# Performance work log

Hardware: AMD Instinct MI355X
Metric: run time of the kernel (lower is better)

## Reference

```python
import jax, jax.numpy as jnp
import numpy as np

N_NODES = 100000
NEG_SLOPE = 0.2  # DGL GATConv default leaky_relu slope


def gat_layer(x, src, dst, W, attn_l, attn_r, bias):
    """One GATConv layer (DGL semantics). x: [N, F_in]; returns [N, H, D]."""
    H, D = attn_l.shape
    z = (x @ W).reshape(-1, H, D)                      # [N, H, D]
    el = jnp.einsum('nhd,hd->nh', z, attn_l)           # [N, H]
    er = jnp.einsum('nhd,hd->nh', z, attn_r)           # [N, H]
    e = jax.nn.leaky_relu(el[src] + er[dst], NEG_SLOPE)  # [E, H]
    # edge-softmax over incoming edges of each dst node
    m = jax.ops.segment_max(e, dst, num_segments=N_NODES)
    m = jnp.where(jnp.isfinite(m), m, 0.0)             # empty segments -> 0
    p = jnp.exp(e - m[dst])                            # [E, H]
    denom = jax.ops.segment_sum(p, dst, num_segments=N_NODES)
    alpha = p / jnp.maximum(denom[dst], 1e-9)          # [E, H]
    msg = z[src] * alpha[:, :, None]                   # [E, H, D]
    out = jax.ops.segment_sum(msg, dst, num_segments=N_NODES)
    return out + bias.reshape(1, H, D)


def setup_inputs() -> dict:
    key = jax.random.key(0)
    ks = jax.random.split(key, 10)
    in_dim, hidden, heads, out_dim, E = 500, 32, 4, 3, 1600000
    features = jax.random.normal(ks[0], (N_NODES, in_dim), dtype=jnp.float32)
    src = jax.random.randint(ks[1], (E,), 0, N_NODES, dtype=jnp.int64 if jax.config.jax_enable_x64 else jnp.int32)
    dst = jnp.sort(jax.random.randint(ks[2], (E,), 0, N_NODES, dtype=src.dtype))
    s1 = 1.0 / np.sqrt(in_dim)
    s2 = 1.0 / np.sqrt(hidden * heads)
    return {
        'features': features, 'src': src, 'dst': dst,
        'W1': jax.random.normal(ks[3], (in_dim, heads * hidden), dtype=jnp.float32) * s1,
        'al1': jax.random.normal(ks[4], (heads, hidden), dtype=jnp.float32) * s1,
        'ar1': jax.random.normal(ks[5], (heads, hidden), dtype=jnp.float32) * s1,
        'b1': jnp.zeros((heads * hidden,), dtype=jnp.float32),
        'W2': jax.random.normal(ks[6], (heads * hidden, out_dim), dtype=jnp.float32) * s2,
        'al2': jax.random.normal(ks[7], (1, out_dim), dtype=jnp.float32) * s2,
        'ar2': jax.random.normal(ks[8], (1, out_dim), dtype=jnp.float32) * s2,
        'b2': jnp.zeros((out_dim,), dtype=jnp.float32),
    }


def reference(features, src, dst, W1, al1, ar1, b1, W2, al2, ar2, b2):
    h = gat_layer(features, src, dst, W1, al1, ar1, b1)   # [N, H, hidden]
    h = jax.nn.elu(h.reshape(h.shape[0], -1))             # [N, H*hidden]
    h = gat_layer(h, src, dst, W2, al2, ar2, b2)          # [N, 1, out_dim]
    return h
```

## Files before the change

kernel.cpp:

```cpp
#include <hip/hip_runtime.h>
#include <hip/hip_fp16.h>
#include <math.h>

#define NNODES 100000
#define NEG_SLOPE 0.2f
#define FIN 500
#define KP 512
#define HID 128
#define NH 4
#define BMG 128

typedef __attribute__((ext_vector_type(8))) _Float16 half8v;
typedef __attribute__((ext_vector_type(4))) float f32x4;

__device__ __forceinline__ float lrelu(float x) { return x > 0.f ? x : NEG_SLOPE * x; }

__device__ __forceinline__ float sel4(float a0, float a1, float a2, float a3, int h) {
  float r = a0;
  r = (h == 1) ? a1 : r;
  r = (h == 2) ? a2 : r;
  r = (h == 3) ? a3 : r;
  return r;
}

__device__ __forceinline__ int tile_off(int col, int slot) {
  return col * 32 + ((slot ^ ((col >> 1) & 3)) << 3);
}

__global__ __launch_bounds__(256) void prep_kernel(const float* __restrict__ W1,
                                                   _Float16* __restrict__ BT_sw,
                                                   const int* __restrict__ dst, int E,
                                                   int* __restrict__ off) {
  int b = blockIdx.x;
  if (b < 256) {
    int p = b * 256 + threadIdx.x;
    int tile = p >> 12;
    int rem = p & 4095;
    int col = rem >> 5;
    int sw = (rem >> 3) & 3;
    int elem = rem & 7;
    int slot = sw ^ ((col >> 1) & 3);
    int k = tile * 32 + slot * 8 + elem;
    float v = (k < FIN) ? W1[k * HID + col] : 0.f;
    BT_sw[p] = (_Float16)v;
  } else {
    int n = (b - 256) * 256 + threadIdx.x;
    if (n > NNODES) return;
    int lo = 0, hi = E;
    while (lo < hi) {
      int mid = (lo + hi) >> 1;
      if (dst[mid] < n) lo = mid + 1; else hi = mid;
    }
    off[n] = lo;
  }
}

__global__ __launch_bounds__(256, 2) void gemm1_mfma_kernel(const float* __restrict__ A,
                                                            const _Float16* __restrict__ BT_sw,
                                                            const float* __restrict__ al,
                                                            const float* __restrict__ ar,
                                                            __half* __restrict__ z1h,
                                                            float* __restrict__ el,
                                                            float* __restrict__ er) {
  __shared__ __align__(16) float As[3][4096];
  __shared__ __align__(16) _Float16 Bsh[3][4096];

  const int t = threadIdx.x;
  const int w = t >> 6, lane = t & 63;
  const int fr = lane & 15, ko = lane >> 4;
  const int bm = blockIdx.x * BMG;

#define STAGE_A(BUF, S)                                                                     \
  do {                                                                                      \
    _Pragma("unroll")                                                                       \
    for (int j = 0; j < 4; j++) {                                                           \
      int c = j * 256 + w * 64 + lane;                                                      \
      int row = c >> 3, sl = c & 7;                                                         \
      int swz = sl ^ (row & 7);                                                             \
      const float* src = A + (size_t)min(bm + row, NNODES - 1) * FIN + (S) * 32 + swz * 4;  \
      __builtin_amdgcn_global_load_lds(                                                     \
          (const __attribute__((address_space(1))) unsigned int*)src,                       \
          (__attribute__((address_space(3))) unsigned int*)&As[BUF][c * 4], 16, 0, 0);      \
    }                                                                                       \
  } while (0)

#define STAGE_B(BUF, S)                                                                     \
  do {                                                                                      \
    _Pragma("unroll")                                                                       \
    for (int j = 0; j < 2; j++) {                                                           \
      int c = j * 256 + w * 64 + lane;                                                      \
      const _Float16* src = BT_sw + (size_t)(S) * 4096 + c * 8;                             \
      __builtin_amdgcn_global_load_lds(                                                     \
          (const __attribute__((address_space(1))) unsigned int*)src,                       \
          (__attribute__((address_space(3))) unsigned int*)&Bsh[BUF][c * 8], 16, 0, 0);     \
    }                                                                                       \
  } while (0)

  f32x4 acc[2][8];
#pragma unroll
  for (int i = 0; i < 2; i++)
#pragma unroll
    for (int j = 0; j < 8; j++) acc[i][j] = (f32x4){0.f, 0.f, 0.f, 0.f};

#define COMPUTE_STEP(BUF)                                                                   \
  do {                                                                                      \
    _Pragma("unroll")                                                                       \
    for (int mi = 0; mi < 2; mi++) {                                                        \
      int row = w * 32 + mi * 16 + fr;                                                      \
      int r7 = row & 7;                                                                     \
      const float* ap = &As[BUF][row * 32];                                                 \
      f32x4 a0 = *(const f32x4*)(ap + (((ko * 2) ^ r7) << 2));                              \
      f32x4 a1 = *(const f32x4*)(ap + (((ko * 2 + 1) ^ r7) << 2));                          \
      half8v af;                                                                            \
      _Pragma("unroll")                                                                     \
      for (int i = 0; i < 4; i++) {                                                         \
        af[i] = (_Float16)a0[i];                                                            \
        af[i + 4] = (_Float16)a1[i];                                                        \
      }                                                                                     \
      _Pragma("unroll")                                                                     \
      for (int ni = 0; ni < 8; ni++) {                                                      \
        half8v bf = *(half8v*)&Bsh[BUF][tile_off(ni * 16 + fr, ko)];                        \
        acc[mi][ni] = __builtin_amdgcn_mfma_f32_16x16x32_f16(af, bf, acc[mi][ni], 0, 0, 0); \
      }                                                                                     \
    }                                                                                       \
  } while (0)

  STAGE_A(0, 0);
  STAGE_B(0, 0);
  STAGE_A(1, 1);
  STAGE_B(1, 1);

#pragma unroll
  for (int s = 0; s < 16; ++s) {
    const int cb = s % 3;
    if (s <= 13) {
      asm volatile("s_waitcnt vmcnt(6)" ::: "memory");
    } else if (s == 14) {
      asm volatile("s_waitcnt vmcnt(2)" ::: "memory");
    } else {
      asm volatile("s_waitcnt vmcnt(0)" ::: "memory");
    }
    __builtin_amdgcn_sched_barrier(0);
    __builtin_amdgcn_s_barrier();
    __builtin_amdgcn_sched_barrier(0);
    if (s + 2 <= 14) {
      STAGE_A((s + 2) % 3, s + 2);
      STAGE_B((s + 2) % 3, s + 2);
    } else if (s + 2 == 15) {
      STAGE_B((s + 2) % 3, 15);
    }
    if (s < 15) {
      COMPUTE_STEP(cb);
    } else {
#pragma unroll
      for (int mi = 0; mi < 2; mi++) {
        int grow = min(bm + w * 32 + mi * 16 + fr, NNODES - 1);
        const float* pa = A + (size_t)grow * FIN;
        half8v af;
#pragma unroll
        for (int i = 0; i < 8; i++) {
          int k0 = 480 + ko * 8 + i;
          af[i] = (_Float16)((k0 < FIN) ? pa[k0] : 0.f);
        }
#pragma unroll
        for (int ni = 0; ni < 8; ni++) {
          half8v bf = *(half8v*)&Bsh[cb][tile_off(ni * 16 + fr, ko)];
          acc[mi][ni] = __builtin_amdgcn_mfma_f32_16x16x32_f16(af, bf, acc[mi][ni], 0, 0, 0);
        }
      }
    }
  }

#undef STAGE_A
#undef STAGE_B
#undef COMPUTE_STEP

  float alv[8], arv[8];
#pragma unroll
  for (int ni = 0; ni < 8; ni++) {
    alv[ni] = al[ni * 16 + fr];
    arv[ni] = ar[ni * 16 + fr];
  }
#pragma unroll
  for (int mi = 0; mi < 2; mi++) {
#pragma unroll
    for (int r = 0; r < 4; r++) {
      int grow = bm + w * 32 + mi * 16 + ko * 4 + r;
      bool ok = grow < NNODES;
      if (ok) {
#pragma unroll
        for (int ni = 0; ni < 8; ni++)
          z1h[(size_t)grow * HID + ni * 16 + fr] = __float2half(acc[mi][ni][r]);
      }
#pragma unroll
      for (int h = 0; h < 4; h++) {
        float cl = acc[mi][2 * h][r] * alv[2 * h] + acc[mi][2 * h + 1][r] * alv[2 * h + 1];
        float cr = acc[mi][2 * h][r] * arv[2 * h] + acc[mi][2 * h + 1][r] * arv[2 * h + 1];
#pragma unroll
        for (int m = 1; m <= 8; m <<= 1) {
          cl += __shfl_xor(cl, m);
          cr += __shfl_xor(cr, m);
        }
        if (fr == 0 && ok) {
          el[grow * NH + h] = cl;
          er[grow * NH + h] = cr;
        }
      }
    }
  }
}

__global__ __launch_bounds__(256) void gat1_agg_kernel(const __half* __restrict__ z1h,
                                                       const float* __restrict__ el,
                                                       const float* __restrict__ er,
                                                       const int* __restrict__ src,
                                                       const int* __restrict__ off,
                                                       const float* __restrict__ b1,
                                                       const float* __restrict__ W2,
                                                       const float* __restrict__ al2,
                                                       const float* __restrict__ ar2,
                                                       float4* __restrict__ z2el,
                                                       float* __restrict__ er2) {
  int wid = threadIdx.x >> 6, lane = threadIdx.x & 63;
  int n = blockIdx.x * 4 + wid;
  if (n >= NNODES) return;
  __shared__ float p_sh[4][64 * 4];

  int start = off[n], end = off[n + 1];
  const float4* el4 = reinterpret_cast<const float4*>(el);
  float4 er4 = reinterpret_cast<const float4*>(er)[n];

  const int g = lane >> 4;
  const int c4 = lane & 15;
  const int headc = c4 >> 2;
  float aA0 = 0.f, aA1 = 0.f, aA2 = 0.f, aA3 = 0.f;
  float aA4 = 0.f, aA5 = 0.f, aA6 = 0.f, aA7 = 0.f;
  float aB0 = 0.f, aB1 = 0.f, aB2 = 0.f, aB3 = 0.f;
  float aB4 = 0.f, aB5 = 0.f, aB6 = 0.f, aB7 = 0.f;
  float d0 = 0.f, d1 = 0.f, d2 = 0.f, d3 = 0.f;

  for (int base = start; base < end; base += 64) {
    int cnt = min(64, end - base);
    int sr = 0;
    float p0 = 0.f, p1 = 0.f, p2 = 0.f, p3 = 0.f;
    if (lane < cnt) {
      sr = src[base + lane];
      float4 x = el4[sr];
      p0 = __expf(lrelu(x.x + er4.x));
      p1 = __expf(lrelu(x.y + er4.y));
      p2 = __expf(lrelu(x.z + er4.z));
      p3 = __expf(lrelu(x.w + er4.w));
      d0 += p0; d1 += p1; d2 += p2; d3 += p3;
    }
    *(float4*)&p_sh[wid][lane * 4] = make_float4(p0, p1, p2, p3);
    __builtin_amdgcn_wave_barrier();
    for (int i = 0; i < cnt; i += 8) {
      int ea = i + g, eb = i + 4 + g;
      bool va_ = ea < cnt, vb_ = eb < cnt;
      int sa = __shfl(sr, va_ ? ea : 0);
      int sb = __shfl(sr, vb_ ? eb : 0);
      float pa = va_ ? p_sh[wid][ea * 4 + headc] : 0.f;
      float pb = vb_ ? p_sh[wid][eb * 4 + headc] : 0.f;
      uint4 ra = reinterpret_cast<const uint4*>(z1h + (size_t)sa * HID)[c4];
      uint4 rb = reinterpret_cast<const uint4*>(z1h + (size_t)sb * HID)[c4];
      float2 va0 = __half22float2(*(__half2*)&ra.x);
      float2 va1 = __half22float2(*(__half2*)&ra.y);
      float2 va2 = __half22float2(*(__half2*)&ra.z);
      float2 va3 = __half22float2(*(__half2*)&ra.w);
      aA0 = fmaf(pa, va0.x, aA0); aA1 = fmaf(pa, va0.y, aA1);
      aA2 = fmaf(pa, va1.x, aA2); aA3 = fmaf(pa, va1.y, aA3);
      aA4 = fmaf(pa, va2.x, aA4); aA5 = fmaf(pa, va2.y, aA5);
      aA6 = fmaf(pa, va3.x, aA6); aA7 = fmaf(pa, va3.y, aA7);
      float2 vb0 = __half22float2(*(__half2*)&rb.x);
      float2 vb1 = __half22float2(*(__half2*)&rb.y);
      float2 vb2 = __half22float2(*(__half2*)&rb.z);
      float2 vb3 = __half22float2(*(__half2*)&rb.w);
      aB0 = fmaf(pb, vb0.x, aB0); aB1 = fmaf(pb, vb0.y, aB1);
      aB2 = fmaf(pb, vb1.x, aB2); aB3 = fmaf(pb, vb1.y, aB3);
      aB4 = fmaf(pb, vb2.x, aB4); aB5 = fmaf(pb, vb2.y, aB5);
      aB6 = fmaf(pb, vb3.x, aB6); aB7 = fmaf(pb, vb3.y, aB7);
    }
    __builtin_amdgcn_wave_barrier();
  }

  float acc0 = aA0 + aB0, acc1 = aA1 + aB1, acc2 = aA2 + aB2, acc3 = aA3 + aB3;
  float acc4 = aA4 + aB4, acc5 = aA5 + aB5, acc6 = aA6 + aB6, acc7 = aA7 + aB7;

#pragma unroll
  for (int msk = 32; msk >= 1; msk >>= 1) {
    d0 += __shfl_xor(d0, msk);
    d1 += __shfl_xor(d1, msk);
    d2 += __shfl_xor(d2, msk);
    d3 += __shfl_xor(d3, msk);
  }
#pragma unroll
  for (int msk = 16; msk <= 32; msk <<= 1) {
    acc0 += __shfl_xor(acc0, msk); acc1 += __shfl_xor(acc1, msk);
    acc2 += __shfl_xor(acc2, msk); acc3 += __shfl_xor(acc3, msk);
    acc4 += __shfl_xor(acc4, msk); acc5 += __shfl_xor(acc5, msk);
    acc6 += __shfl_xor(acc6, msk); acc7 += __shfl_xor(acc7, msk);
  }

  if (g == 0) {
    float dh = sel4(d0, d1, d2, d3, headc);
    float inv = 1.f / fmaxf(dh, 1e-9f);
    float4 ba = reinterpret_cast<const float4*>(b1)[c4 * 2];
    float4 bb = reinterpret_cast<const float4*>(b1)[c4 * 2 + 1];
    float v0 = acc0 * inv + ba.x, v1 = acc1 * inv + ba.y;
    float v2 = acc2 * inv + ba.z, v3 = acc3 * inv + ba.w;
    float v4 = acc4 * inv + bb.x, v5 = acc5 * inv + bb.y;
    float v6 = acc6 * inv + bb.z, v7 = acc7 * inv + bb.w;
    v0 = v0 > 0.f ? v0 : __expf(v0) - 1.f;
    v1 = v1 > 0.f ? v1 : __expf(v1) - 1.f;
    v2 = v2 > 0.f ? v2 : __expf(v2) - 1.f;
    v3 = v3 > 0.f ? v3 : __expf(v3) - 1.f;
    v4 = v4 > 0.f ? v4 : __expf(v4) - 1.f;
    v5 = v5 > 0.f ? v5 : __expf(v5) - 1.f;
    v6 = v6 > 0.f ? v6 : __expf(v6) - 1.f;
    v7 = v7 > 0.f ? v7 : __expf(v7) - 1.f;
    const float* Wp = W2 + c4 * 8 * 3;
    float q0 = v0 * Wp[0] + v1 * Wp[3] + v2 * Wp[6] + v3 * Wp[9] +
               v4 * Wp[12] + v5 * Wp[15] + v6 * Wp[18] + v7 * Wp[21];
    float q1 = v0 * Wp[1] + v1 * Wp[4] + v2 * Wp[7] + v3 * Wp[10] +
               v4 * Wp[13] + v5 * Wp[16] + v6 * Wp[19] + v7 * Wp[22];
    float q2 = v0 * Wp[2] + v1 * Wp[5] + v2 * Wp[8] + v3 * Wp[11] +
               v4 * Wp[14] + v5 * Wp[17] + v6 * Wp[20] + v7 * Wp[23];
#pragma unroll
    for (int msk = 8; msk >= 1; msk >>= 1) {
      q0 += __shfl_xor(q0, msk);
      q1 += __shfl_xor(q1, msk);
      q2 += __shfl_xor(q2, msk);
    }
    if (c4 == 0) {
      z2el[n] = make_float4(q0, q1, q2, q0 * al2[0] + q1 * al2[1] + q2 * al2[2]);
      er2[n] = q0 * ar2[0] + q1 * ar2[1] + q2 * ar2[2];
    }
  }
}

__global__ __launch_bounds__(256) void gat2_agg_kernel(const float4* __restrict__ z2el,
                                                       const float* __restrict__ er2,
                                                       const int* __restrict__ src,
                                                       const int* __restrict__ off,
                                                       const float* __restrict__ b2,
                                                       float* __restrict__ out) {
  int wid = threadIdx.x >> 6, lane = threadIdx.x & 63;
  int n = blockIdx.x * 4 + wid;
  if (n >= NNODES) return;
  int start = off[n], end = off[n + 1];
  float ern = er2[n];
  float dA = 0.f, x0 = 0.f, x1 = 0.f, x2 = 0.f;
  float dB = 0.f, y0 = 0.f, y1 = 0.f, y2 = 0.f;
  int base = start + lane;
  for (; base + 64 < end; base += 128) {
    float4 za = z2el[src[base]];
    float4 zb = z2el[src[base + 64]];
    float pa = __expf(lrelu(za.w + ern));
    float pb = __expf(lrelu(zb.w + ern));
    dA += pa; dB += pb;
    x0 = fmaf(pa, za.x, x0); x1 = fmaf(pa, za.y, x1); x2 = fmaf(pa, za.z, x2);
    y0 = fmaf(pb, zb.x, y0); y1 = fmaf(pb, zb.y, y1); y2 = fmaf(pb, zb.z, y2);
  }
  if (base < end) {
    float4 za = z2el[src[base]];
    float pa = __expf(lrelu(za.w + ern));
    dA += pa;
    x0 = fmaf(pa, za.x, x0); x1 = fmaf(pa, za.y, x1); x2 = fmaf(pa, za.z, x2);
  }
  float d = dA + dB, a0 = x0 + y0, a1 = x1 + y1, a2 = x2 + y2;
#pragma unroll
  for (int msk = 32; msk >= 1; msk >>= 1) {
    a0 += __shfl_xor(a0, msk);
    a1 += __shfl_xor(a1, msk);
    a2 += __shfl_xor(a2, msk);
    d += __shfl_xor(d, msk);
  }
  if (lane == 0) {
    float inv = 1.f / fmaxf(d, 1e-9f);
    out[n * 3 + 0] = a0 * inv + b2[0];
    out[n * 3 + 1] = a1 * inv + b2[1];
    out[n * 3 + 2] = a2 * inv + b2[2];
  }
}

extern "C" void kernel_launch(void* const* d_in, const int* in_sizes, int n_in,
                              void* d_out, int out_size, void* d_ws, size_t ws_size,
                              hipStream_t stream) {
  const float* features = (const float*)d_in[0];
  const int* src = (const int*)d_in[1];
  const int* dst = (const int*)d_in[2];
  const float* W1 = (const float*)d_in[3];
  const float* al1 = (const float*)d_in[4];
  const float* ar1 = (const float*)d_in[5];
  const float* b1 = (const float*)d_in[6];
  const float* W2 = (const float*)d_in[7];
  const float* al2 = (const float*)d_in[8];
  const float* ar2 = (const float*)d_in[9];
  const float* b2 = (const float*)d_in[10];
  float* out = (float*)d_out;
  int E = in_sizes[1];

  char* ws = (char*)d_ws;
  size_t o = 0;
  __half* z1h = (__half*)(ws + o);  o += (size_t)NNODES * HID * 2;
  float* el1 = (float*)(ws + o);    o += (size_t)NNODES * NH * 4;
  float* er1 = (float*)(ws + o);    o += (size_t)NNODES * NH * 4;
  float4* z2el = (float4*)(ws + o); o += (size_t)NNODES * 16;
  float* er2 = (float*)(ws + o);    o += (size_t)NNODES * 4;
  _Float16* BT_sw = (_Float16*)(ws + o); o += (size_t)HID * KP * 2;
  int* off = (int*)(ws + o);        o += (size_t)(NNODES + 1) * 4;

  prep_kernel<<<256 + (NNODES + 1 + 255) / 256, 256, 0, stream>>>(W1, BT_sw, dst, E, off);
  gemm1_mfma_kernel<<<(NNODES + BMG - 1) / BMG, 256, 0, stream>>>(features, BT_sw, al1, ar1,
                                                                  z1h, el1, er1);
  gat1_agg_kernel<<<(NNODES + 3) / 4, 256, 0, stream>>>(z1h, el1, er1, src, off, b1,
                                                        W2, al2, ar2, z2el, er2);
  gat2_agg_kernel<<<(NNODES + 3) / 4, 256, 0, stream>>>(z2el, er2, src, off, b2, out);
}
```

Baseline: 171.3 us.

## Stage GEMM1 A tile through registers as fp16 in LDS, raise occupancy

The A operand of the first GEMM was copied to LDS as fp32 with direct global-to-LDS loads and converted to fp16 by every consumer wave at each step. Now each thread loads its row segment into registers, converts it to fp16 once, and writes it to LDS in the same swizzled tile layout as B. The tail K step is handled through the same path with zero padding, and launch bounds move to three blocks per CU since LDS use drops. This removes the repeated conversions and halves A's LDS footprint, at the cost of extra registers held in flight and an extra LDS write and wait before each barrier.

```diff
diff --git a/kernel.cpp b/kernel.cpp
--- a/kernel.cpp
+++ b/kernel.cpp
@@ -55,14 +55,14 @@
   }
 }
 
-__global__ __launch_bounds__(256, 2) void gemm1_mfma_kernel(const float* __restrict__ A,
+__global__ __launch_bounds__(256, 3) void gemm1_mfma_kernel(const float* __restrict__ A,
                                                             const _Float16* __restrict__ BT_sw,
                                                             const float* __restrict__ al,
                                                             const float* __restrict__ ar,
                                                             __half* __restrict__ z1h,
                                                             float* __restrict__ el,
                                                             float* __restrict__ er) {
-  __shared__ __align__(16) float As[3][4096];
+  __shared__ __align__(16) _Float16 Ash[3][4096];
   __shared__ __align__(16) _Float16 Bsh[3][4096];
 
   const int t = threadIdx.x;
@@ -70,18 +70,49 @@
   const int fr = lane & 15, ko = lane >> 4;
   const int bm = blockIdx.x * BMG;
 
-#define STAGE_A(BUF, S)                                                                     \
-  do {                                                                                      \
-    _Pragma("unroll")                                                                       \
-    for (int j = 0; j < 4; j++) {                                                           \
-      int c = j * 256 + w * 64 + lane;                                                      \
-      int row = c >> 3, sl = c & 7;                                                         \
-      int swz = sl ^ (row & 7);                                                             \
-      const float* src = A + (size_t)min(bm + row, NNODES - 1) * FIN + (S) * 32 + swz * 4;  \
-      __builtin_amdgcn_global_load_lds(                                                     \
-          (const __attribute__((address_space(1))) unsigned int*)src,                       \
-          (__attribute__((address_space(3))) unsigned int*)&As[BUF][c * 4], 16, 0, 0);      \
-    }                                                                                       \
+  const int rowl = t >> 1, khalf = t & 1;
+  const int arow = min(bm + rowl, NNODES - 1);
+  const float* pArow = A + (size_t)arow * FIN;
+  const int aoff0 = tile_off(rowl, khalf * 2);
+  const int aoff1 = tile_off(rowl, khalf * 2 + 1);
+
+#define LOAD_A(S, R0, R1, R2, R3)                                  \
+  do {                                                             \
+    const float* pa = pArow + (S) * 32 + khalf * 16;               \
+    R0 = *(const f32x4*)(pa);                                      \
+    R1 = *(const f32x4*)(pa + 4);                                  \
+    R2 = *(const f32x4*)(pa + 8);                                  \
+    R3 = *(const f32x4*)(pa + 12);                                 \
+  } while (0)
+
+#define LOAD_A_EDGE(R0, R1, R2, R3)                                  \
+  do {                                                               \
+    const float* pa = pArow + 480 + khalf * 16;                      \
+    int _e1 = khalf ? 0 : 4, _e2 = khalf ? 0 : 8, _e3 = khalf ? 0 : 12; \
+    R0 = *(const f32x4*)(pa);                                        \
+    R1 = *(const f32x4*)(pa + _e1);                                  \
+    R2 = *(const f32x4*)(pa + _e2);                                  \
+    R3 = *(const f32x4*)(pa + _e3);                                  \
+  } while (0)
+
+#define CONV_WRITE(BUF, S, R0, R1, R2, R3)                         \
+  do {                                                             \
+    half8v h0, h1;                                                 \
+    _Pragma("unroll")                                              \
+    for (int i = 0; i < 4; i++) {                                  \
+      h0[i] = (_Float16)R0[i];                                     \
+      h0[i + 4] = (_Float16)R1[i];                                 \
+      h1[i] = (_Float16)R2[i];                                     \
+      h1[i + 4] = (_Float16)R3[i];                                 \
+    }                                                              \
+    if ((S) == 15 && khalf) {                                      \
+      _Pragma("unroll")                                            \
+      for (int i = 0; i < 4; i++) h0[i + 4] = (_Float16)0.f;       \
+      _Pragma("unroll")                                            \
+      for (int i = 0; i < 8; i++) h1[i] = (_Float16)0.f;           \
+    }                                                              \
+    *(half8v*)&Ash[BUF][aoff0] = h0;                               \
+    *(half8v*)&Ash[BUF][aoff1] = h1;                               \
   } while (0)
 
 #define STAGE_B(BUF, S)                                                                     \
@@ -106,17 +137,7 @@
   do {                                                                                      \
     _Pragma("unroll")                                                                       \
     for (int mi = 0; mi < 2; mi++) {                                                        \
-      int row = w * 32 + mi * 16 + fr;                                                      \
-      int r7 = row & 7;                                                                     \
-      const float* ap = &As[BUF][row * 32];                                                 \
-      f32x4 a0 = *(const f32x4*)(ap + (((ko * 2) ^ r7) << 2));                              \
-      f32x4 a1 = *(const f32x4*)(ap + (((ko * 2 + 1) ^ r7) << 2));                          \
-      half8v af;                                                                            \
-      _Pragma("unroll")                                                                     \
-      for (int i = 0; i < 4; i++) {                                                         \
-        af[i] = (_Float16)a0[i];                                                            \
-        af[i + 4] = (_Float16)a1[i];                                                        \
-      }                                                                                     \
+      half8v af = *(half8v*)&Ash[BUF][tile_off(w * 32 + mi * 16 + fr, ko)];                 \
       _Pragma("unroll")                                                                     \
       for (int ni = 0; ni < 8; ni++) {                                                      \
         half8v bf = *(half8v*)&Bsh[BUF][tile_off(ni * 16 + fr, ko)];                        \
@@ -125,53 +146,48 @@
     }                                                                                       \
   } while (0)
 
-  STAGE_A(0, 0);
+  f32x4 e0, e1, e2, e3, o0, o1, o2, o3;
+
+  LOAD_A(0, e0, e1, e2, e3);
   STAGE_B(0, 0);
-  STAGE_A(1, 1);
+  LOAD_A(1, o0, o1, o2, o3);
   STAGE_B(1, 1);
 
 #pragma unroll
   for (int s = 0; s < 16; ++s) {
     const int cb = s % 3;
-    if (s <= 13) {
+    if (s <= 14) {
       asm volatile("s_waitcnt vmcnt(6)" ::: "memory");
-    } else if (s == 14) {
-      asm volatile("s_waitcnt vmcnt(2)" ::: "memory");
     } else {
       asm volatile("s_waitcnt vmcnt(0)" ::: "memory");
     }
+    __builtin_amdgcn_sched_barrier(0);
+    if ((s & 1) == 0) {
+      CONV_WRITE(cb, s, e0, e1, e2, e3);
+    } else {
+      CONV_WRITE(cb, s, o0, o1, o2, o3);
+    }
+    asm volatile("s_waitcnt lgkmcnt(0)" ::: "memory");
     __builtin_amdgcn_sched_barrier(0);
     __builtin_amdgcn_s_barrier();
     __builtin_amdgcn_sched_barrier(0);
     if (s + 2 <= 14) {
-      STAGE_A((s + 2) % 3, s + 2);
+      if ((s & 1) == 0) {
+        LOAD_A(s + 2, e0, e1, e2, e3);
+      } else {
+        LOAD_A(s + 2, o0, o1, o2, o3);
+      }
       STAGE_B((s + 2) % 3, s + 2);
     } else if (s + 2 == 15) {
+      LOAD_A_EDGE(o0, o1, o2, o3);
       STAGE_B((s + 2) % 3, 15);
     }
-    if (s < 15) {
-      COMPUTE_STEP(cb);
-    } else {
-#pragma unroll
-      for (int mi = 0; mi < 2; mi++) {
-        int grow = min(bm + w * 32 + mi * 16 + fr, NNODES - 1);
-        const float* pa = A + (size_t)grow * FIN;
-        half8v af;
-#pragma unroll
-        for (int i = 0; i < 8; i++) {
-          int k0 = 480 + ko * 8 + i;
-          af[i] = (_Float16)((k0 < FIN) ? pa[k0] : 0.f);
-        }
-#pragma unroll
-        for (int ni = 0; ni < 8; ni++) {
-          half8v bf = *(half8v*)&Bsh[cb][tile_off(ni * 16 + fr, ko)];
-          acc[mi][ni] = __builtin_amdgcn_mfma_f32_16x16x32_f16(af, bf, acc[mi][ni], 0, 0, 0);
-        }
-      }
-    }
-  }
-
-#undef STAGE_A
+    COMPUTE_STEP(cb);
+  }
+
+#undef LOAD_A
+#undef LOAD_A_EDGE
+#undef CONV_WRITE
 #undef STAGE_B
 #undef COMPUTE_STEP
 
```

Result: no change. 171.5 us, median of 2 (+0.1%).
